# Performance work log

Hardware: AMD Instinct MI355X
Metric: run time of the kernel (lower is better)

Reference implementation:

```python
import jax, jax.numpy as jnp
import numpy as np

H = 4
N = 1024
E = 4096
LE = 16384
FN = 128
FE = 64
FNO = 128
FEO = 64


def _lin(x, W, b):
    # torch nn.Linear: y = x @ W.T + b, W is [out, in]
    return x @ W.T + b


def setup_inputs() -> dict:
    key = jax.random.key(0)
    ks = jax.random.split(key, 24)
    s = 0.05
    inp = {}
    inp["node_inputs"] = jax.random.normal(ks[0], (N, FN), jnp.float32)
    inp["edge_inputs"] = jax.random.normal(ks[1], (E, FE), jnp.float32)
    inp["src"] = jax.random.randint(ks[2], (E,), 0, N, jnp.int32)
    inp["dst"] = jax.random.randint(ks[3], (E,), 0, N, jnp.int32)
    inp["lg_src"] = jax.random.randint(ks[4], (LE,), 0, E, jnp.int32)
    inp["lg_dst"] = jax.random.randint(ks[5], (LE,), 0, E, jnp.int32)
    # projection linear weights (torch Linear layout [out, in])
    inp["nqW"] = jax.random.normal(ks[6], (H * FN, FN), jnp.float32) * s
    inp["nqb"] = jax.random.normal(ks[7], (H * FN,), jnp.float32) * s
    inp["nkW"] = jax.random.normal(ks[8], (H, FN), jnp.float32) * s
    inp["nkb"] = jax.random.normal(ks[9], (H,), jnp.float32) * s
    inp["nvW"] = jax.random.normal(ks[10], (H * FN, FN), jnp.float32) * s
    inp["nvb"] = jax.random.normal(ks[11], (H * FN,), jnp.float32) * s
    inp["eqW"] = jax.random.normal(ks[12], (H * FE, FE), jnp.float32) * s
    inp["eqb"] = jax.random.normal(ks[13], (H * FE,), jnp.float32) * s
    inp["ekW"] = jax.random.normal(ks[14], (H, FE), jnp.float32) * s
    inp["ekb"] = jax.random.normal(ks[15], (H,), jnp.float32) * s
    inp["evW"] = jax.random.normal(ks[16], (H * FE, FE), jnp.float32) * s
    inp["evb"] = jax.random.normal(ks[17], (H * FE,), jnp.float32) * s
    # convolution output linears
    inp["ncW"] = jax.random.normal(ks[18], (FNO, FN), jnp.float32) * s
    inp["ncb"] = jax.random.normal(ks[19], (FNO,), jnp.float32) * s
    inp["ecW"] = jax.random.normal(ks[20], (FEO, FE), jnp.float32) * s
    inp["ecb"] = jax.random.normal(ks[21], (FEO,), jnp.float32) * s
    return inp


def reference(node_inputs, edge_inputs, src, dst, lg_src, lg_dst,
              nqW, nqb, nkW, nkb, nvW, nvb,
              eqW, eqb, ekW, ekb, evW, evb,
              ncW, ncb, ecW, ecb):
    n, fn = node_inputs.shape
    e, fe = edge_inputs.shape
    # per-head Q/K/V projections; .view(H, -1, F) == row-major reshape
    nq = _lin(node_inputs, nqW, nqb).reshape(H, -1, fn)   # [H,N,FN]
    nk = _lin(node_inputs, nkW, nkb).reshape(H, -1, 1)    # [H,N,1]
    nv = _lin(node_inputs, nvW, nvb).reshape(H, -1, fn)   # [H,N,FN]
    eq = _lin(edge_inputs, eqW, eqb).reshape(H, -1, fe)   # [H,E,FE]
    ek = _lin(edge_inputs, ekW, ekb).reshape(H, -1, 1)    # [H,E,1]
    ev = _lin(edge_inputs, evW, evb).reshape(H, -1, fe)   # [H,E,FE]
    # self attention: softmax(Q @ Q^T @ K, dim=1); associate as Q @ (Q^T K)
    node_sa = jax.nn.softmax(nq @ (jnp.swapaxes(nq, -1, -2) @ nk), axis=1)  # [H,N,1]
    edge_sa = jax.nn.softmax(eq @ (jnp.swapaxes(eq, -1, -2) @ ek), axis=1)  # [H,E,1]
    # vectorized edge-indexed scatter of attention scores into dense projections
    node_proj = jnp.zeros((H, n, n), node_inputs.dtype).at[:, src, dst].set(edge_sa[:, :, 0])
    conn = dst[lg_src]  # g.find_edges(source)[1]: destination node of edge lg_src
    edge_proj = jnp.zeros((H, e, e), edge_inputs.dtype).at[:, lg_src, lg_dst].set(node_sa[:, conn, 0])
    # dense adjacency matrices
    A = jnp.zeros((n, n), node_inputs.dtype).at[src, dst].set(1.0)
    Alg = jnp.zeros((e, e), edge_inputs.dtype).at[lg_src, lg_dst].set(1.0)
    # 'sum' aggregation: (attn_proj * A) @ value, then Linear + relu
    node_out = jax.nn.relu(_lin((node_proj * A) @ nv, ncW, ncb))   # [H,N,FNO]
    edge_out = jax.nn.relu(_lin((edge_proj * Alg) @ ev, ecW, ecb)) # [H,E,FEO]
    return (node_out, edge_out)
```

## Files before the change

### kernel.cpp

```cpp
#include <hip/hip_runtime.h>

#define H_ 4
#define N_ 1024
#define E_ 4096
#define LE_ 16384
#define FN_ 128
#define FE_ 64
#define HTN_ 16384
#define HTE_ 65536
#define CAP_ 32

struct P {
  const float *Xn, *Xe;
  const int *src, *dst, *lgs, *lgd;
  const float *nqW, *nqb, *nkW, *nkb, *nvW, *nvb;
  const float *eqW, *eqb, *ekW, *ekb, *evW, *evb;
  const float *ncW, *ncb, *ecW, *ecb;
  float *out;
  float *NV, *EV, *nsa, *esa;
  int *hkN, *hvN, *hkE, *hvE;
  int *cntN, *cntE, *listN, *listE;
};

__device__ __forceinline__ unsigned hashN(int key) {
  return (((unsigned)key * 2654435761u) >> 16) & (HTN_ - 1);
}
__device__ __forceinline__ unsigned hashE(int key) {
  return (((unsigned)key * 2654435761u) >> 16) & (HTE_ - 1);
}

template<int K, bool RELU>
__device__ void gemm_tile(const float* __restrict__ X, const float* __restrict__ W,
                          const float* __restrict__ b, float* __restrict__ C,
                          int O, int r0, int o0, float* smem, int t) {
  float* Xs = smem;
  float* Ws = smem + 2048;
  const int tn = t & 15, tm = t >> 4;
  float acc[4][4] = {};
  for (int k0 = 0; k0 < K; k0 += 32) {
#pragma unroll
    for (int ph = 0; ph < 2; ++ph) {
      int i4 = t + ph * 256;
      int m = i4 >> 3;
      int k4 = (i4 & 7) << 2;
      int m4 = m >> 2, ml = m & 3;
      float4 vx = *(const float4*)&X[(r0 + m) * K + k0 + k4];
      float4 vw = *(const float4*)&W[(o0 + m) * K + k0 + k4];
      Xs[(k4 + 0) * 64 + ((m4 ^ ((k4 + 0) & 15)) << 2) + ml] = vx.x;
      Xs[(k4 + 1) * 64 + ((m4 ^ ((k4 + 1) & 15)) << 2) + ml] = vx.y;
      Xs[(k4 + 2) * 64 + ((m4 ^ ((k4 + 2) & 15)) << 2) + ml] = vx.z;
      Xs[(k4 + 3) * 64 + ((m4 ^ ((k4 + 3) & 15)) << 2) + ml] = vx.w;
      Ws[(k4 + 0) * 64 + ((m4 ^ ((k4 + 0) & 15)) << 2) + ml] = vw.x;
      Ws[(k4 + 1) * 64 + ((m4 ^ ((k4 + 1) & 15)) << 2) + ml] = vw.y;
      Ws[(k4 + 2) * 64 + ((m4 ^ ((k4 + 2) & 15)) << 2) + ml] = vw.z;
      Ws[(k4 + 3) * 64 + ((m4 ^ ((k4 + 3) & 15)) << 2) + ml] = vw.w;
    }
    __syncthreads();
#pragma unroll
    for (int k = 0; k < 32; ++k) {
      float4 a = *(const float4*)&Xs[k * 64 + ((tm ^ (k & 15)) << 2)];
      float4 b4 = *(const float4*)&Ws[k * 64 + ((tn ^ (k & 15)) << 2)];
      acc[0][0] += a.x * b4.x; acc[0][1] += a.x * b4.y; acc[0][2] += a.x * b4.z; acc[0][3] += a.x * b4.w;
      acc[1][0] += a.y * b4.x; acc[1][1] += a.y * b4.y; acc[1][2] += a.y * b4.z; acc[1][3] += a.y * b4.w;
      acc[2][0] += a.z * b4.x; acc[2][1] += a.z * b4.y; acc[2][2] += a.z * b4.z; acc[2][3] += a.z * b4.w;
      acc[3][0] += a.w * b4.x; acc[3][1] += a.w * b4.y; acc[3][2] += a.w * b4.z; acc[3][3] += a.w * b4.w;
    }
    __syncthreads();
  }
  float4 bv = *(const float4*)&b[o0 + tn * 4];
#pragma unroll
  for (int i = 0; i < 4; ++i) {
    float4 o;
    o.x = acc[i][0] + bv.x; o.y = acc[i][1] + bv.y;
    o.z = acc[i][2] + bv.z; o.w = acc[i][3] + bv.w;
    if (RELU) {
      o.x = fmaxf(o.x, 0.f); o.y = fmaxf(o.y, 0.f);
      o.z = fmaxf(o.z, 0.f); o.w = fmaxf(o.w, 0.f);
    }
    *(float4*)&C[(r0 + tm * 4 + i) * O + o0 + tn * 4] = o;
  }
}

__global__ __launch_bounds__(1024) void kA(P p) {
  __shared__ float smem[16384];
  const int tid = threadIdx.x;
  const int bid = blockIdx.x;

  if (bid >= 28) {
    const int gg = (bid - 28) * 4 + (tid >> 8);
    const int ts_ = tid & 255;
    float* gsm = smem + (tid >> 8) * 4096;
    if (gg % 3 == 0) {
      const int tile = gg / 3;
      gemm_tile<128, false>(p.Xn, p.nvW, p.nvb, p.NV, 512,
                            (tile >> 3) * 64, (tile & 7) * 64, gsm, ts_);
    } else {
      const int tile = gg - gg / 3 - 1;
      gemm_tile<64, false>(p.Xe, p.evW, p.evb, p.EV, 256,
                           (tile >> 2) * 64, (tile & 3) * 64, gsm, ts_);
      __syncthreads(); __syncthreads(); __syncthreads(); __syncthreads();
    }
    return;
  }

  if (bid >= 8) {
    int idx = (bid - 8) * 1024 + tid;
    if (idx < E_) {
      int key = p.src[idx] * N_ + p.dst[idx];
      unsigned slot = hashN(key);
      while (true) {
        int prev = atomicCAS(&p.hkN[slot], -1, key);
        if (prev == -1 || prev == key) break;
        slot = (slot + 1) & (HTN_ - 1);
      }
      atomicMax(&p.hvN[slot], idx);
    } else if (idx < E_ + LE_) {
      int l = idx - E_;
      int key = p.lgs[l] * E_ + p.lgd[l];
      unsigned slot = hashE(key);
      while (true) {
        int prev = atomicCAS(&p.hkE[slot], -1, key);
        if (prev == -1 || prev == key) break;
        slot = (slot + 1) & (HTE_ - 1);
      }
      atomicMax(&p.hvE[slot], l);
    }
    return;
  }

  float4* accs = (float4*)smem;
  float* red = smem + 4096;
  float* ys  = smem + 5120;
  float* ts  = smem + 5632;
  float* zs  = smem + 5760;
  float* ds  = smem + 6288;
  float* sig = smem + 6292;
  float* Ks  = smem + 6304;

  if (bid < 4) {
    const int h = bid;
    const int r0 = h * 256;
    float* wkw = Ks + 1024;
    for (int i = tid; i < 512; i += 1024) wkw[i] = p.nkW[i];
    __syncthreads();
    {
      const int rl = tid >> 2, c = tid & 3;
      const float4* x4 = (const float4*)(p.Xn + (r0 + rl) * FN_);
      const float4* w4 = (const float4*)(wkw + c * FN_);
      float acc = p.nkb[c];
      for (int k = 0; k < 32; ++k) {
        float4 x = x4[k], w = w4[k];
        acc += x.x * w.x + x.y * w.y + x.z * w.z + x.w * w.w;
      }
      Ks[tid] = acc;
    }
    __syncthreads();
    {
      int g = tid & 127, q = tid >> 7;
      const float4* Ks4 = (const float4*)Ks;
      float a0 = 0, a1 = 0, a2 = 0, a3 = 0;
      for (int jj = 0; jj < 32; ++jj) {
        int lr = q * 32 + jj;
        float x = p.Xn[(r0 + lr) * FN_ + g];
        float4 k = Ks4[lr];
        a0 += x * k.x; a1 += x * k.y; a2 += x * k.z; a3 += x * k.w;
      }
      accs[tid] = make_float4(a0, a1, a2, a3);
    }
    __syncthreads();
    for (int off = 512; off >= 128; off >>= 1) {
      if (tid < off) {
        float4 a = accs[tid], b = accs[tid + off];
        accs[tid] = make_float4(a.x + b.x, a.y + b.y, a.z + b.z, a.w + b.w);
      }
      __syncthreads();
    }
    if (tid < 128) {
      float4 a = accs[tid];
      ys[tid * 4 + 0] = a.x; ys[tid * 4 + 1] = a.y;
      ys[tid * 4 + 2] = a.z; ys[tid * 4 + 3] = a.w;
    }
    if (tid >= 128 && tid < 160) {
      int t2 = tid - 128, c = t2 & 3, part = t2 >> 2;
      float s = 0.f;
      for (int j = 0; j < 32; ++j) s += Ks[(part * 32 + j) * 4 + c];
      red[t2] = s;
    }
    __syncthreads();
    if (tid < 4) { float s = 0.f; for (int q = 0; q < 8; ++q) s += red[q * 4 + tid]; sig[tid] = s; }
    __syncthreads();
    if (tid < 512) {
      const float4* w4 = (const float4*)(p.nqW + tid * FN_);
      int c = tid >> 7;
      float s = 0.f;
      for (int g4 = 0; g4 < 32; ++g4) {
        float4 w = w4[g4];
        s += w.x * ys[(g4 * 4 + 0) * 4 + c] + w.y * ys[(g4 * 4 + 1) * 4 + c]
           + w.z * ys[(g4 * 4 + 2) * 4 + c] + w.w * ys[(g4 * 4 + 3) * 4 + c];
      }
      red[tid] = s;
    }
    __syncthreads();
    if (tid < 128) {
      float s = red[tid] + red[128 + tid] + red[256 + tid] + red[384 + tid];
      float bb = 0.f;
      for (int c = 0; c < 4; ++c) bb += p.nqb[c * 128 + tid] * sig[c];
      ts[tid] = s + bb;
    }
    __syncthreads();
    if (tid < 512) {
      int c = tid >> 7, g = tid & 127;
      float s = 0.f;
      for (int f = 0; f < 128; ++f) s += p.nqW[(c * 128 + f) * 128 + g] * ts[f];
      zs[c * 132 + g] = s;
    }
    if (tid >= 512 && tid < 516) {
      int c = tid - 512;
      float s = 0.f;
      for (int f = 0; f < 128; ++f) s += p.nqb[c * 128 + f] * ts[f];
      ds[c] = s;
    }
    __syncthreads();
    float sc;
    {
      int c = tid & 3, j = tid >> 2;
      const float4* x4 = (const float4*)(p.Xn + (r0 + j) * FN_);
      const float* z = zs + c * 132;
      float s = ds[c];
      for (int g4 = 0; g4 < 32; ++g4) {
        float4 x = x4[g4];
        s += x.x * z[g4 * 4] + x.y * z[g4 * 4 + 1] + x.z * z[g4 * 4 + 2] + x.w * z[g4 * 4 + 3];
      }
      sc = s;
    }
    red[tid] = sc;
    __syncthreads();
    for (int off = 512; off > 0; off >>= 1) {
      if (tid < off) red[tid] = fmaxf(red[tid], red[tid + off]);
      __syncthreads();
    }
    float m = red[0];
    __syncthreads();
    float e = expf(sc - m);
    red[tid] = e;
    __syncthreads();
    for (int off = 512; off > 0; off >>= 1) {
      if (tid < off) red[tid] += red[tid + off];
      __syncthreads();
    }
    p.nsa[h * N_ + tid] = e / red[0];
  } else {
    const int h = bid - 4;
    const int r0 = h * 1024;
    float* wkw = Ks + 4096;
    for (int i = tid; i < 256; i += 1024) wkw[i] = p.ekW[i];
    __syncthreads();
    {
      const float4* x4 = (const float4*)(p.Xe + (r0 + tid) * FE_);
      const float4* w0 = (const float4*)wkw;
      const float4* w1 = (const float4*)(wkw + 64);
      const float4* w2 = (const float4*)(wkw + 128);
      const float4* w3 = (const float4*)(wkw + 192);
      float a0 = p.ekb[0], a1 = p.ekb[1], a2 = p.ekb[2], a3 = p.ekb[3];
      for (int k = 0; k < 16; ++k) {
        float4 x = x4[k];
        float4 u0 = w0[k], u1 = w1[k], u2 = w2[k], u3 = w3[k];
        a0 += x.x * u0.x + x.y * u0.y + x.z * u0.z + x.w * u0.w;
        a1 += x.x * u1.x + x.y * u1.y + x.z * u1.z + x.w * u1.w;
        a2 += x.x * u2.x + x.y * u2.y + x.z * u2.z + x.w * u2.w;
        a3 += x.x * u3.x + x.y * u3.y + x.z * u3.z + x.w * u3.w;
      }
      Ks[tid * 4 + 0] = a0; Ks[tid * 4 + 1] = a1;
      Ks[tid * 4 + 2] = a2; Ks[tid * 4 + 3] = a3;
    }
    __syncthreads();
    {
      int g = tid & 63, q = tid >> 6;
      const float4* Ks4 = (const float4*)Ks;
      float a0 = 0, a1 = 0, a2 = 0, a3 = 0;
      for (int jj = 0; jj < 64; ++jj) {
        int lr = q * 64 + jj;
        float x = p.Xe[(r0 + lr) * FE_ + g];
        float4 k = Ks4[lr];
        a0 += x * k.x; a1 += x * k.y; a2 += x * k.z; a3 += x * k.w;
      }
      accs[tid] = make_float4(a0, a1, a2, a3);
    }
    __syncthreads();
    for (int off = 512; off >= 64; off >>= 1) {
      if (tid < off) {
        float4 a = accs[tid], b = accs[tid + off];
        accs[tid] = make_float4(a.x + b.x, a.y + b.y, a.z + b.z, a.w + b.w);
      }
      __syncthreads();
    }
    if (tid < 64) {
      float4 a = accs[tid];
      ys[tid * 4 + 0] = a.x; ys[tid * 4 + 1] = a.y;
      ys[tid * 4 + 2] = a.z; ys[tid * 4 + 3] = a.w;
    }
    if (tid >= 128 && tid < 160) {
      int t2 = tid - 128, c = t2 & 3, part = t2 >> 2;
      float s = 0.f;
      for (int j = 0; j < 128; ++j) s += Ks[(part * 128 + j) * 4 + c];
      red[t2] = s;
    }
    __syncthreads();
    if (tid < 4) { float s = 0.f; for (int q = 0; q < 8; ++q) s += red[q * 4 + tid]; sig[tid] = s; }
    __syncthreads();
    if (tid < 256) {
      const float4* w4 = (const float4*)(p.eqW + tid * FE_);
      int c = tid >> 6;
      float s = 0.f;
      for (int g4 = 0; g4 < 16; ++g4) {
        float4 w = w4[g4];
        s += w.x * ys[(g4 * 4 + 0) * 4 + c] + w.y * ys[(g4 * 4 + 1) * 4 + c]
           + w.z * ys[(g4 * 4 + 2) * 4 + c] + w.w * ys[(g4 * 4 + 3) * 4 + c];
      }
      red[tid] = s;
    }
    __syncthreads();
    if (tid < 64) {
      float s = red[tid] + red[64 + tid] + red[128 + tid] + red[192 + tid];
      float bb = 0.f;
      for (int c = 0; c < 4; ++c) bb += p.eqb[c * 64 + tid] * sig[c];
      ts[tid] = s + bb;
    }
    __syncthreads();
    if (tid < 256) {
      int c = tid >> 6, g = tid & 63;
      float s = 0.f;
      for (int f = 0; f < 64; ++f) s += p.eqW[(c * 64 + f) * 64 + g] * ts[f];
      zs[c * 132 + g] = s;
    }
    if (tid >= 256 && tid < 260) {
      int c = tid - 256;
      float s = 0.f;
      for (int f = 0; f < 64; ++f) s += p.eqb[c * 64 + f] * ts[f];
      ds[c] = s;
    }
    __syncthreads();
    float s4[4];
    {
      const float4* x4 = (const float4*)(p.Xe + (r0 + tid) * FE_);
      s4[0] = ds[0]; s4[1] = ds[1]; s4[2] = ds[2]; s4[3] = ds[3];
      for (int g4 = 0; g4 < 16; ++g4) {
        float4 x = x4[g4];
#pragma unroll
        for (int c = 0; c < 4; ++c) {
          const float* z = zs + c * 132 + g4 * 4;
          s4[c] += x.x * z[0] + x.y * z[1] + x.z * z[2] + x.w * z[3];
        }
      }
    }
    float lm = fmaxf(fmaxf(s4[0], s4[1]), fmaxf(s4[2], s4[3]));
    red[tid] = lm;
    __syncthreads();
    for (int off = 512; off > 0; off >>= 1) {
      if (tid < off) red[tid] = fmaxf(red[tid], red[tid + off]);
      __syncthreads();
    }
    float m = red[0];
    __syncthreads();
    float e0 = expf(s4[0] - m), e1 = expf(s4[1] - m);
    float e2 = expf(s4[2] - m), e3 = expf(s4[3] - m);
    red[tid] = e0 + e1 + e2 + e3;
    __syncthreads();
    for (int off = 512; off > 0; off >>= 1) {
      if (tid < off) red[tid] += red[tid + off];
      __syncthreads();
    }
    float inv = 1.f / red[0];
    ((float4*)(p.esa + h * E_))[tid] = make_float4(e0 * inv, e1 * inv, e2 * inv, e3 * inv);
  }
}

__global__ __launch_bounds__(256) void kB(P p) {
  int idx = blockIdx.x * 256 + threadIdx.x;
  if (idx < E_) {
    int e = idx;
    int s = p.src[e], d = p.dst[e];
    int key = s * N_ + d;
    unsigned slot = hashN(key);
    while (p.hkN[slot] != key) slot = (slot + 1) & (HTN_ - 1);
    if (p.hvN[slot] != e) return;
    int pos = atomicAdd(&p.cntN[s], 1) & (CAP_ - 1);
    p.listN[s * CAP_ + pos] = (d << 12) | e;
  } else {
    int l = idx - E_;
    int j = p.lgs[l], c = p.lgd[l];
    int key = j * E_ + c;
    unsigned slot = hashE(key);
    while (p.hkE[slot] != key) slot = (slot + 1) & (HTE_ - 1);
    if (p.hvE[slot] != l) return;
    int pos = atomicAdd(&p.cntE[j], 1) & (CAP_ - 1);
    p.listE[j * CAP_ + pos] = c;
  }
}

__global__ __launch_bounds__(256) void kC(P p) {
  __shared__ float smem[10240];
  const int t = threadIdx.x, bid = blockIdx.x;
  float* Xs = smem;
  float* Ws = smem + 8192;
  const int tn = t & 15, tm = t >> 4;

  if (bid < 128) {
    const int rt = bid >> 1, o0 = (bid & 1) << 6;
    const int h = rt >> 4, p0 = (rt & 15) << 6;
    {
      const int m = t >> 2, q = t & 3;
      const int s = p0 + m;
      const int deg = min(p.cntN[s], CAP_);
      float4 acc[8];
#pragma unroll
      for (int f = 0; f < 8; ++f) acc[f] = make_float4(0.f, 0.f, 0.f, 0.f);
      const float4* NV4 = (const float4*)p.NV + (h << 15);
      const float* esah = p.esa + h * E_;
      for (int i = 0; i < deg; ++i) {
        int pk = p.listN[s * CAP_ + i];
        int e = pk & (E_ - 1), d = pk >> 12;
        float a = esah[e];
        const float4* v4 = NV4 + (d << 5);
#pragma unroll
        for (int f = 0; f < 8; ++f) {
          float4 v = v4[q + (f << 2)];
          acc[f].x += a * v.x; acc[f].y += a * v.y;
          acc[f].z += a * v.z; acc[f].w += a * v.w;
        }
      }
      const int m4 = m >> 2, ml = m & 3;
#pragma unroll
      for (int f = 0; f < 8; ++f) {
        int k4 = (q + (f << 2)) << 2;
        Xs[(k4 + 0) * 64 + ((m4 ^ ((k4 + 0) & 15)) << 2) + ml] = acc[f].x;
        Xs[(k4 + 1) * 64 + ((m4 ^ ((k4 + 1) & 15)) << 2) + ml] = acc[f].y;
        Xs[(k4 + 2) * 64 + ((m4 ^ ((k4 + 2) & 15)) << 2) + ml] = acc[f].z;
        Xs[(k4 + 3) * 64 + ((m4 ^ ((k4 + 3) & 15)) << 2) + ml] = acc[f].w;
      }
    }
    float c16[4][4] = {};
    for (int k0 = 0; k0 < 128; k0 += 32) {
#pragma unroll
      for (int ph = 0; ph < 2; ++ph) {
        int i4 = t + ph * 256;
        int mw = i4 >> 3, k4 = (i4 & 7) << 2;
        int w4i = mw >> 2, wl = mw & 3;
        float4 vw = *(const float4*)&p.ncW[(o0 + mw) * 128 + k0 + k4];
        Ws[(k4 + 0) * 64 + ((w4i ^ ((k4 + 0) & 15)) << 2) + wl] = vw.x;
        Ws[(k4 + 1) * 64 + ((w4i ^ ((k4 + 1) & 15)) << 2) + wl] = vw.y;
        Ws[(k4 + 2) * 64 + ((w4i ^ ((k4 + 2) & 15)) << 2) + wl] = vw.z;
        Ws[(k4 + 3) * 64 + ((w4i ^ ((k4 + 3) & 15)) << 2) + wl] = vw.w;
      }
      __syncthreads();
#pragma unroll
      for (int kk = 0; kk < 32; ++kk) {
        int k = k0 + kk;
        float4 a = *(const float4*)&Xs[k * 64 + ((tm ^ (k & 15)) << 2)];
        float4 b4 = *(const float4*)&Ws[kk * 64 + ((tn ^ (kk & 15)) << 2)];
        c16[0][0] += a.x * b4.x; c16[0][1] += a.x * b4.y; c16[0][2] += a.x * b4.z; c16[0][3] += a.x * b4.w;
        c16[1][0] += a.y * b4.x; c16[1][1] += a.y * b4.y; c16[1][2] += a.y * b4.z; c16[1][3] += a.y * b4.w;
        c16[2][0] += a.z * b4.x; c16[2][1] += a.z * b4.y; c16[2][2] += a.z * b4.z; c16[2][3] += a.z * b4.w;
        c16[3][0] += a.w * b4.x; c16[3][1] += a.w * b4.y; c16[3][2] += a.w * b4.z; c16[3][3] += a.w * b4.w;
      }
      __syncthreads();
    }
    float4 bv = *(const float4*)&p.ncb[o0 + tn * 4];
#pragma unroll
    for (int i = 0; i < 4; ++i) {
      float4 o;
      o.x = fmaxf(c16[i][0] + bv.x, 0.f); o.y = fmaxf(c16[i][1] + bv.y, 0.f);
      o.z = fmaxf(c16[i][2] + bv.z, 0.f); o.w = fmaxf(c16[i][3] + bv.w, 0.f);
      *(float4*)&p.out[((h << 10) + p0 + tm * 4 + i) * 128 + o0 + tn * 4] = o;
    }
  } else {
    const int rt = bid - 128;
    const int h = rt >> 6, j0 = (rt & 63) << 6;
    {
      const int m = t >> 2, q = t & 3;
      const int j = j0 + m;
      const int deg = min(p.cntE[j], CAP_);
      float4 acc[4];
#pragma unroll
      for (int f = 0; f < 4; ++f) acc[f] = make_float4(0.f, 0.f, 0.f, 0.f);
      const float4* EV4 = (const float4*)p.EV + (h << 16);
      for (int i = 0; i < deg; ++i) {
        int c = p.listE[j * CAP_ + i];
        const float4* v4 = EV4 + (c << 4);
#pragma unroll
        for (int f = 0; f < 4; ++f) {
          float4 v = v4[q + (f << 2)];
          acc[f].x += v.x; acc[f].y += v.y; acc[f].z += v.z; acc[f].w += v.w;
        }
      }
      float a = p.nsa[h * N_ + p.dst[j]];
      const int m4 = m >> 2, ml = m & 3;
#pragma unroll
      for (int f = 0; f < 4; ++f) {
        int k4 = (q + (f << 2)) << 2;
        Xs[(k4 + 0) * 64 + ((m4 ^ ((k4 + 0) & 15)) << 2) + ml] = a * acc[f].x;
        Xs[(k4 + 1) * 64 + ((m4 ^ ((k4 + 1) & 15)) << 2) + ml] = a * acc[f].y;
        Xs[(k4 + 2) * 64 + ((m4 ^ ((k4 + 2) & 15)) << 2) + ml] = a * acc[f].z;
        Xs[(k4 + 3) * 64 + ((m4 ^ ((k4 + 3) & 15)) << 2) + ml] = a * acc[f].w;
      }
    }
    float c16[4][4] = {};
    for (int k0 = 0; k0 < 64; k0 += 32) {
#pragma unroll
      for (int ph = 0; ph < 2; ++ph) {
        int i4 = t + ph * 256;
        int mw = i4 >> 3, k4 = (i4 & 7) << 2;
        int w4i = mw >> 2, wl = mw & 3;
        float4 vw = *(const float4*)&p.ecW[mw * 64 + k0 + k4];
        Ws[(k4 + 0) * 64 + ((w4i ^ ((k4 + 0) & 15)) << 2) + wl] = vw.x;
        Ws[(k4 + 1) * 64 + ((w4i ^ ((k4 + 1) & 15)) << 2) + wl] = vw.y;
        Ws[(k4 + 2) * 64 + ((w4i ^ ((k4 + 2) & 15)) << 2) + wl] = vw.z;
        Ws[(k4 + 3) * 64 + ((w4i ^ ((k4 + 3) & 15)) << 2) + wl] = vw.w;
      }
      __syncthreads();
#pragma unroll
      for (int kk = 0; kk < 32; ++kk) {
        int k = k0 + kk;
        float4 a = *(const float4*)&Xs[k * 64 + ((tm ^ (k & 15)) << 2)];
        float4 b4 = *(const float4*)&Ws[kk * 64 + ((tn ^ (kk & 15)) << 2)];
        c16[0][0] += a.x * b4.x; c16[0][1] += a.x * b4.y; c16[0][2] += a.x * b4.z; c16[0][3] += a.x * b4.w;
        c16[1][0] += a.y * b4.x; c16[1][1] += a.y * b4.y; c16[1][2] += a.y * b4.z; c16[1][3] += a.y * b4.w;
        c16[2][0] += a.z * b4.x; c16[2][1] += a.z * b4.y; c16[2][2] += a.z * b4.z; c16[2][3] += a.z * b4.w;
        c16[3][0] += a.w * b4.x; c16[3][1] += a.w * b4.y; c16[3][2] += a.w * b4.z; c16[3][3] += a.w * b4.w;
      }
      __syncthreads();
    }
    float4 bv = *(const float4*)&p.ecb[tn * 4];
    float* out2 = p.out + 524288;
#pragma unroll
    for (int i = 0; i < 4; ++i) {
      float4 o;
      o.x = fmaxf(c16[i][0] + bv.x, 0.f); o.y = fmaxf(c16[i][1] + bv.y, 0.f);
      o.z = fmaxf(c16[i][2] + bv.z, 0.f); o.w = fmaxf(c16[i][3] + bv.w, 0.f);
      *(float4*)&out2[((h << 12) + j0 + tm * 4 + i) * 64 + tn * 4] = o;
    }
  }
}

extern "C" void kernel_launch(void* const* d_in, const int* in_sizes, int n_in,
                              void* d_out, int out_size, void* d_ws, size_t ws_size,
                              hipStream_t stream) {
  P p;
  p.Xn  = (const float*)d_in[0];
  p.Xe  = (const float*)d_in[1];
  p.src = (const int*)d_in[2];
  p.dst = (const int*)d_in[3];
  p.lgs = (const int*)d_in[4];
  p.lgd = (const int*)d_in[5];
  p.nqW = (const float*)d_in[6];  p.nqb = (const float*)d_in[7];
  p.nkW = (const float*)d_in[8];  p.nkb = (const float*)d_in[9];
  p.nvW = (const float*)d_in[10]; p.nvb = (const float*)d_in[11];
  p.eqW = (const float*)d_in[12]; p.eqb = (const float*)d_in[13];
  p.ekW = (const float*)d_in[14]; p.ekb = (const float*)d_in[15];
  p.evW = (const float*)d_in[16]; p.evb = (const float*)d_in[17];
  p.ncW = (const float*)d_in[18]; p.ncb = (const float*)d_in[19];
  p.ecW = (const float*)d_in[20]; p.ecb = (const float*)d_in[21];
  p.out = (float*)d_out;

  float* f = (float*)d_ws;
  p.NV   = f; f += N_ * H_ * FN_;
  p.EV   = f; f += E_ * H_ * FE_;
  p.nsa  = f; f += H_ * N_;
  p.esa  = f; f += H_ * E_;
  int* ip = (int*)f;
  p.hkN  = ip; ip += HTN_;
  p.hvN  = ip; ip += HTN_;
  p.hkE  = ip; ip += HTE_;
  p.hvE  = ip; ip += HTE_;
  p.cntN = ip; ip += N_;
  p.cntE = ip; ip += E_;
  p.listN = ip; ip += N_ * CAP_;
  p.listE = ip; ip += E_ * CAP_;

  hipMemsetAsync(p.hkN, 0xFF, (size_t)(2 * HTN_ + 2 * HTE_) * sizeof(int), stream);
  hipMemsetAsync(p.cntN, 0, (size_t)(N_ + E_) * sizeof(int), stream);

  kA<<<124, 1024, 0, stream>>>(p);
  kB<<<80, 256, 0, stream>>>(p);
  kC<<<384, 256, 0, stream>>>(p);
}
```

Before: 151.6 us.

## Replace global hash-table dedup with per-block shared-memory adjacency build

Removes the global hash-table insert in kA, the separate kB list-building kernel and both memsets. Each kC block now scans the full edge or line-graph edge array and builds its own 64-row adjacency lists in shared memory. Duplicate (src,dst) pairs are resolved there by an O(deg^2) scan that keeps the last writer for nodes and the first occurrence for edges. This cuts two memsets and one kernel launch plus global atomics, at the cost of every block redundantly scanning E or LE indices.

```diff
diff --git a/kernel.cpp b/kernel.cpp
--- a/kernel.cpp
+++ b/kernel.cpp
@@ -6,8 +6,6 @@
 #define LE_ 16384
 #define FN_ 128
 #define FE_ 64
-#define HTN_ 16384
-#define HTE_ 65536
 #define CAP_ 32
 
 struct P {
@@ -18,16 +16,7 @@
   const float *ncW, *ncb, *ecW, *ecb;
   float *out;
   float *NV, *EV, *nsa, *esa;
-  int *hkN, *hvN, *hkE, *hvE;
-  int *cntN, *cntE, *listN, *listE;
 };
-
-__device__ __forceinline__ unsigned hashN(int key) {
-  return (((unsigned)key * 2654435761u) >> 16) & (HTN_ - 1);
-}
-__device__ __forceinline__ unsigned hashE(int key) {
-  return (((unsigned)key * 2654435761u) >> 16) & (HTE_ - 1);
-}
 
 template<int K, bool RELU>
 __device__ void gemm_tile(const float* __restrict__ X, const float* __restrict__ W,
@@ -86,8 +75,8 @@
   const int tid = threadIdx.x;
   const int bid = blockIdx.x;
 
-  if (bid >= 28) {
-    const int gg = (bid - 28) * 4 + (tid >> 8);
+  if (bid >= 8) {
+    const int gg = (bid - 8) * 4 + (tid >> 8);
     const int ts_ = tid & 255;
     float* gsm = smem + (tid >> 8) * 4096;
     if (gg % 3 == 0) {
@@ -99,31 +88,6 @@
       gemm_tile<64, false>(p.Xe, p.evW, p.evb, p.EV, 256,
                            (tile >> 2) * 64, (tile & 3) * 64, gsm, ts_);
       __syncthreads(); __syncthreads(); __syncthreads(); __syncthreads();
-    }
-    return;
-  }
-
-  if (bid >= 8) {
-    int idx = (bid - 8) * 1024 + tid;
-    if (idx < E_) {
-      int key = p.src[idx] * N_ + p.dst[idx];
-      unsigned slot = hashN(key);
-      while (true) {
-        int prev = atomicCAS(&p.hkN[slot], -1, key);
-        if (prev == -1 || prev == key) break;
-        slot = (slot + 1) & (HTN_ - 1);
-      }
-      atomicMax(&p.hvN[slot], idx);
-    } else if (idx < E_ + LE_) {
-      int l = idx - E_;
-      int key = p.lgs[l] * E_ + p.lgd[l];
-      unsigned slot = hashE(key);
-      while (true) {
-        int prev = atomicCAS(&p.hkE[slot], -1, key);
-        if (prev == -1 || prev == key) break;
-        slot = (slot + 1) & (HTE_ - 1);
-      }
-      atomicMax(&p.hvE[slot], l);
     }
     return;
   }
@@ -375,31 +339,10 @@
   }
 }
 
-__global__ __launch_bounds__(256) void kB(P p) {
-  int idx = blockIdx.x * 256 + threadIdx.x;
-  if (idx < E_) {
-    int e = idx;
-    int s = p.src[e], d = p.dst[e];
-    int key = s * N_ + d;
-    unsigned slot = hashN(key);
-    while (p.hkN[slot] != key) slot = (slot + 1) & (HTN_ - 1);
-    if (p.hvN[slot] != e) return;
-    int pos = atomicAdd(&p.cntN[s], 1) & (CAP_ - 1);
-    p.listN[s * CAP_ + pos] = (d << 12) | e;
-  } else {
-    int l = idx - E_;
-    int j = p.lgs[l], c = p.lgd[l];
-    int key = j * E_ + c;
-    unsigned slot = hashE(key);
-    while (p.hkE[slot] != key) slot = (slot + 1) & (HTE_ - 1);
-    if (p.hvE[slot] != l) return;
-    int pos = atomicAdd(&p.cntE[j], 1) & (CAP_ - 1);
-    p.listE[j * CAP_ + pos] = c;
-  }
-}
-
 __global__ __launch_bounds__(256) void kC(P p) {
   __shared__ float smem[10240];
+  __shared__ int cnt_s[64];
+  __shared__ int list_s[64 * CAP_];
   const int t = threadIdx.x, bid = blockIdx.x;
   float* Xs = smem;
   float* Ws = smem + 8192;
@@ -408,17 +351,33 @@
   if (bid < 128) {
     const int rt = bid >> 1, o0 = (bid & 1) << 6;
     const int h = rt >> 4, p0 = (rt & 15) << 6;
+    if (t < 64) cnt_s[t] = 0;
+    __syncthreads();
+    for (int i = t; i < E_; i += 256) {
+      int ls = p.src[i] - p0;
+      if ((unsigned)ls < 64u) {
+        int pos = atomicAdd(&cnt_s[ls], 1) & (CAP_ - 1);
+        list_s[ls * CAP_ + pos] = (p.dst[i] << 12) | i;
+      }
+    }
+    __syncthreads();
     {
       const int m = t >> 2, q = t & 3;
-      const int s = p0 + m;
-      const int deg = min(p.cntN[s], CAP_);
+      const int deg = min(cnt_s[m], CAP_);
+      const int* lst = list_s + m * CAP_;
       float4 acc[8];
 #pragma unroll
       for (int f = 0; f < 8; ++f) acc[f] = make_float4(0.f, 0.f, 0.f, 0.f);
       const float4* NV4 = (const float4*)p.NV + (h << 15);
       const float* esah = p.esa + h * E_;
       for (int i = 0; i < deg; ++i) {
-        int pk = p.listN[s * CAP_ + i];
+        int pk = lst[i];
+        bool win = true;
+        for (int i2 = 0; i2 < deg; ++i2) {
+          int pk2 = lst[i2];
+          if ((pk2 >> 12) == (pk >> 12) && pk2 > pk) win = false;
+        }
+        if (!win) continue;
         int e = pk & (E_ - 1), d = pk >> 12;
         float a = esah[e];
         const float4* v4 = NV4 + (d << 5);
@@ -476,16 +435,30 @@
   } else {
     const int rt = bid - 128;
     const int h = rt >> 6, j0 = (rt & 63) << 6;
+    if (t < 64) cnt_s[t] = 0;
+    __syncthreads();
+    for (int i = t; i < LE_; i += 256) {
+      int lj = p.lgs[i] - j0;
+      if ((unsigned)lj < 64u) {
+        int pos = atomicAdd(&cnt_s[lj], 1) & (CAP_ - 1);
+        list_s[lj * CAP_ + pos] = p.lgd[i];
+      }
+    }
+    __syncthreads();
     {
       const int m = t >> 2, q = t & 3;
-      const int j = j0 + m;
-      const int deg = min(p.cntE[j], CAP_);
+      const int deg = min(cnt_s[m], CAP_);
+      const int* lst = list_s + m * CAP_;
       float4 acc[4];
 #pragma unroll
       for (int f = 0; f < 4; ++f) acc[f] = make_float4(0.f, 0.f, 0.f, 0.f);
       const float4* EV4 = (const float4*)p.EV + (h << 16);
       for (int i = 0; i < deg; ++i) {
-        int c = p.listE[j * CAP_ + i];
+        int c = lst[i];
+        bool first = true;
+        for (int i2 = 0; i2 < i; ++i2)
+          if (lst[i2] == c) first = false;
+        if (!first) continue;
         const float4* v4 = EV4 + (c << 4);
 #pragma unroll
         for (int f = 0; f < 4; ++f) {
@@ -493,7 +466,7 @@
           acc[f].x += v.x; acc[f].y += v.y; acc[f].z += v.z; acc[f].w += v.w;
         }
       }
-      float a = p.nsa[h * N_ + p.dst[j]];
+      float a = p.nsa[h * N_ + p.dst[j0 + m]];
       const int m4 = m >> 2, ml = m & 3;
 #pragma unroll
       for (int f = 0; f < 4; ++f) {
@@ -567,20 +540,7 @@
   p.EV   = f; f += E_ * H_ * FE_;
   p.nsa  = f; f += H_ * N_;
   p.esa  = f; f += H_ * E_;
-  int* ip = (int*)f;
-  p.hkN  = ip; ip += HTN_;
-  p.hvN  = ip; ip += HTN_;
-  p.hkE  = ip; ip += HTE_;
-  p.hvE  = ip; ip += HTE_;
-  p.cntN = ip; ip += N_;
-  p.cntE = ip; ip += E_;
-  p.listN = ip; ip += N_ * CAP_;
-  p.listE = ip; ip += E_ * CAP_;
-
-  hipMemsetAsync(p.hkN, 0xFF, (size_t)(2 * HTN_ + 2 * HTE_) * sizeof(int), stream);
-  hipMemsetAsync(p.cntN, 0, (size_t)(N_ + E_) * sizeof(int), stream);
-
-  kA<<<124, 1024, 0, stream>>>(p);
-  kB<<<80, 256, 0, stream>>>(p);
+
+  kA<<<104, 1024, 0, stream>>>(p);
   kC<<<384, 256, 0, stream>>>(p);
 }
```

Result: slower. 159.7 us (+5.3%).
